# Kernel tuning notes

Hardware: AMD Instinct MI355X
Metric: run time of the kernel (lower is better)

## Reference

```python
import jax, jax.numpy as jnp
import numpy as np

B, N, D = 2, 512, 64
LN_EPS = 1e-5
NEG_SLOPE = 0.01  # torch nn.LeakyReLU default


def _layer_norm(x, g, b):
    m = jnp.mean(x, axis=-1, keepdims=True)
    v = jnp.mean(jnp.square(x - m), axis=-1, keepdims=True)
    return (x - m) * jax.lax.rsqrt(v + LN_EPS) * g + b


def setup_inputs() -> dict:
    key = jax.random.key(0)
    k0, k1, k2 = jax.random.split(key, 3)
    return {
        "ua": jax.random.normal(k0, (B, N, D), dtype=jnp.float32),
        "iid": jax.random.normal(k1, (B, 1, 1, D), dtype=jnp.float32),
        "ln_g": jnp.ones((D,), dtype=jnp.float32),
        "ln_b": jnp.zeros((D,), dtype=jnp.float32),
        "w_att": (jax.random.normal(k2, (3 * D, 1), dtype=jnp.float32)
                  / np.sqrt(3 * D).astype(np.float32)),
        "b_att": jnp.zeros((1,), dtype=jnp.float32),
    }


def reference(ua, iid, ln_g, ln_b, w_att, b_att):
    b, n, d = ua.shape
    # all-pairs expand: query[b,i,j,:] = ua[b,i,:], key[b,i,j,:] = ua[b,j,:]
    query = jnp.broadcast_to(ua[:, :, None, :], (b, n, n, d))
    key = jnp.broadcast_to(ua[:, None, :, :], (b, n, n, d))
    value = query * key
    iid_e = jnp.broadcast_to(iid, (b, n, n, d))
    wq = _layer_norm(query, ln_g, ln_b)
    wk = _layer_norm(key, ln_g, ln_b)
    wiid = _layer_norm(iid_e, ln_g, ln_b)
    qk = jnp.concatenate((wq, wk, wiid), axis=-1)  # [b,n,n,3d]
    qk = qk @ w_att + b_att                        # [b,n,n,1]
    qk = jax.nn.leaky_relu(qk, NEG_SLOPE)
    # dropout in eval mode -> identity
    scores = jnp.squeeze(qk, axis=-1)              # [b,n,n]
    alphas = jax.nn.softmax(scores, axis=-1)       # softmax over keys j
    alphas = jnp.broadcast_to(alphas[..., None], value.shape)
    return (alphas, value)
```

## Files before the change

kernel.cpp:

```cpp
#include <hip/hip_runtime.h>

#define BB 2
#define NN 512
#define DD 64
#define LN_EPS 1e-5f
#define NEG_SLOPE 0.01f

typedef float f32x4 __attribute__((ext_vector_type(4)));

__device__ __forceinline__ float wave_reduce_sum(float v) {
    #pragma unroll
    for (int off = 32; off >= 1; off >>= 1)
        v += __shfl_xor(v, off, 64);
    return v;
}

__device__ __forceinline__ float wave_reduce_max(float v) {
    #pragma unroll
    for (int off = 32; off >= 1; off >>= 1)
        v = fmaxf(v, __shfl_xor(v, off, 64));
    return v;
}

__global__ __launch_bounds__(64) void precompute_kernel(
    const float* __restrict__ ua,
    const float* __restrict__ iid,
    const float* __restrict__ ln_g,
    const float* __restrict__ ln_b,
    const float* __restrict__ w_att,
    const float* __restrict__ b_att,
    float* __restrict__ sq,
    float* __restrict__ sk,
    float* __restrict__ cb) {
    const int bid = blockIdx.x;
    const int lane = threadIdx.x;

    const float g = ln_g[lane];
    const float bet = ln_b[lane];

    if (bid < BB * NN) {
        float x = ua[bid * DD + lane];
        float m = wave_reduce_sum(x) * (1.0f / DD);
        float xc = x - m;
        float var = wave_reduce_sum(xc * xc) * (1.0f / DD);
        float r = rsqrtf(var + LN_EPS);
        float w = xc * r * g + bet;
        float s1 = wave_reduce_sum(w * w_att[lane]);
        float s2 = wave_reduce_sum(w * w_att[DD + lane]);
        if (lane == 0) {
            sq[bid] = s1;
            sk[bid] = s2;
        }
    } else {
        int b = bid - BB * NN;
        float x = iid[b * DD + lane];
        float m = wave_reduce_sum(x) * (1.0f / DD);
        float xc = x - m;
        float var = wave_reduce_sum(xc * xc) * (1.0f / DD);
        float r = rsqrtf(var + LN_EPS);
        float w = xc * r * g + bet;
        float s3 = wave_reduce_sum(w * w_att[2 * DD + lane]);
        if (lane == 0) {
            cb[b] = s3 + b_att[0];
        }
    }
}

__global__ __launch_bounds__(256) void write_kernel(
    const float* __restrict__ ua,
    const float* __restrict__ sq,
    const float* __restrict__ sk,
    const float* __restrict__ cb,
    float* __restrict__ out0,
    float* __restrict__ out1) {
    __shared__ float alpha_sh[256];
    __shared__ float red_mx[4];
    __shared__ float red_sm[4];

    const int bid2 = blockIdx.x;
    const int row  = bid2 >> 1;
    const int half = bid2 & 1;
    const int b = row >> 9;
    const int i = row & (NN - 1);
    const int tid = threadIdx.x;

    const float sqi = sq[row];
    const float c = cb[b];

    float s0 = sqi + sk[b * NN + tid] + c;
    float s1 = sqi + sk[b * NN + tid + 256] + c;
    s0 = fmaxf(s0, NEG_SLOPE * s0);
    s1 = fmaxf(s1, NEG_SLOPE * s1);

    float mx = fmaxf(s0, s1);
    mx = wave_reduce_max(mx);
    const int wid = tid >> 6;
    if ((tid & 63) == 0) red_mx[wid] = mx;
    __syncthreads();
    mx = fmaxf(fmaxf(red_mx[0], red_mx[1]), fmaxf(red_mx[2], red_mx[3]));

    float e0 = __expf(s0 - mx);
    float e1 = __expf(s1 - mx);
    float sm = wave_reduce_sum(e0 + e1);
    if ((tid & 63) == 0) red_sm[wid] = sm;
    __syncthreads();
    sm = red_sm[0] + red_sm[1] + red_sm[2] + red_sm[3];
    const float inv = 1.0f / sm;

    alpha_sh[tid] = (half ? e1 : e0) * inv;
    __syncthreads();

    const f32x4* __restrict__ uaB = (const f32x4*)(ua + (size_t)b * NN * DD);
    const f32x4* __restrict__ uaH = uaB + (size_t)half * 256 * 16;

    f32x4* __restrict__ o0 =
        (f32x4*)(out0 + (size_t)row * NN * DD + (size_t)half * 256 * DD);
    f32x4* __restrict__ o1 =
        (f32x4*)(out1 + (size_t)row * NN * DD + (size_t)half * 256 * DD);

    if (tid < 128) {
        const int l = tid;
        #pragma unroll 4
        for (int k = 0; k < 32; ++k) {
            const int idx = l + k * 128;
            const float a = alpha_sh[idx >> 4];
            f32x4 av;
            av.x = a; av.y = a; av.z = a; av.w = a;
            o0[idx] = av;
        }
    } else {
        const int l = tid - 128;
        const f32x4 ui = uaB[(size_t)i * 16 + (l & 15)];
        #pragma unroll 4
        for (int k = 0; k < 32; ++k) {
            const int idx = l + k * 128;
            const f32x4 uj = uaH[idx];
            o1[idx] = ui * uj;
        }
    }
}

extern "C" void kernel_launch(void* const* d_in, const int* in_sizes, int n_in,
                              void* d_out, int out_size, void* d_ws, size_t ws_size,
                              hipStream_t stream) {
    const float* ua    = (const float*)d_in[0];
    const float* iid   = (const float*)d_in[1];
    const float* ln_g  = (const float*)d_in[2];
    const float* ln_b  = (const float*)d_in[3];
    const float* w_att = (const float*)d_in[4];
    const float* b_att = (const float*)d_in[5];

    float* out0 = (float*)d_out;
    float* out1 = out0 + (size_t)BB * NN * NN * DD;

    float* sq = (float*)d_ws;
    float* sk = sq + BB * NN;
    float* cb = sk + BB * NN;

    precompute_kernel<<<BB * NN + BB, 64, 0, stream>>>(ua, iid, ln_g, ln_b,
                                                       w_att, b_att, sq, sk, cb);
    write_kernel<<<BB * NN * 2, 256, 0, stream>>>(ua, sq, sk, cb, out0, out1);
}
```

Before: 50.48 us.

## Fold LayerNorm precompute into value-writing kernel and split alpha writes out

The small per-row LayerNorm/score precompute is merged into a new value kernel that also writes the query*key value output with all 256 threads. The alpha softmax broadcast moves to a separate second kernel that writes only out0, again using all 256 threads. This is meant to overlap the tiny precompute with the bulk value stores and to keep each kernel's store loop uniform instead of split between thread halves. Total output traffic is unchanged, and the precompute branch makes the first wave of each block slightly unbalanced.

Result: faster. 49.04 us (median of 2 runs) (-2.9%).

```diff
diff --git a/kernel.cpp b/kernel.cpp
--- a/kernel.cpp
+++ b/kernel.cpp
@@ -22,7 +22,7 @@
     return v;
 }
 
-__global__ __launch_bounds__(64) void precompute_kernel(
+__global__ __launch_bounds__(256) void value_kernel(
     const float* __restrict__ ua,
     const float* __restrict__ iid,
     const float* __restrict__ ln_g,
@@ -31,57 +31,75 @@
     const float* __restrict__ b_att,
     float* __restrict__ sq,
     float* __restrict__ sk,
-    float* __restrict__ cb) {
-    const int bid = blockIdx.x;
-    const int lane = threadIdx.x;
+    float* __restrict__ cb,
+    float* __restrict__ out1) {
+    const int bid2 = blockIdx.x;
+    const int tid = threadIdx.x;
 
-    const float g = ln_g[lane];
-    const float bet = ln_b[lane];
+    if (tid < 64 && bid2 < BB * NN + BB) {
+        const int lane = tid;
+        const float g = ln_g[lane];
+        const float bet = ln_b[lane];
+        if (bid2 < BB * NN) {
+            float x = ua[bid2 * DD + lane];
+            float m = wave_reduce_sum(x) * (1.0f / DD);
+            float xc = x - m;
+            float var = wave_reduce_sum(xc * xc) * (1.0f / DD);
+            float r = rsqrtf(var + LN_EPS);
+            float w = xc * r * g + bet;
+            float s1 = wave_reduce_sum(w * w_att[lane]);
+            float s2 = wave_reduce_sum(w * w_att[DD + lane]);
+            if (lane == 0) {
+                sq[bid2] = s1;
+                sk[bid2] = s2;
+            }
+        } else {
+            int b = bid2 - BB * NN;
+            float x = iid[b * DD + lane];
+            float m = wave_reduce_sum(x) * (1.0f / DD);
+            float xc = x - m;
+            float var = wave_reduce_sum(xc * xc) * (1.0f / DD);
+            float r = rsqrtf(var + LN_EPS);
+            float w = xc * r * g + bet;
+            float s3 = wave_reduce_sum(w * w_att[2 * DD + lane]);
+            if (lane == 0) {
+                cb[b] = s3 + b_att[0];
+            }
+        }
+    }
 
-    if (bid < BB * NN) {
-        float x = ua[bid * DD + lane];
-        float m = wave_reduce_sum(x) * (1.0f / DD);
-        float xc = x - m;
-        float var = wave_reduce_sum(xc * xc) * (1.0f / DD);
-        float r = rsqrtf(var + LN_EPS);
-        float w = xc * r * g + bet;
-        float s1 = wave_reduce_sum(w * w_att[lane]);
-        float s2 = wave_reduce_sum(w * w_att[DD + lane]);
-        if (lane == 0) {
-            sq[bid] = s1;
-            sk[bid] = s2;
-        }
-    } else {
-        int b = bid - BB * NN;
-        float x = iid[b * DD + lane];
-        float m = wave_reduce_sum(x) * (1.0f / DD);
-        float xc = x - m;
-        float var = wave_reduce_sum(xc * xc) * (1.0f / DD);
-        float r = rsqrtf(var + LN_EPS);
-        float w = xc * r * g + bet;
-        float s3 = wave_reduce_sum(w * w_att[2 * DD + lane]);
-        if (lane == 0) {
-            cb[b] = s3 + b_att[0];
-        }
+    const int row = bid2 >> 1;
+    const int half = bid2 & 1;
+    const int b = row >> 9;
+    const int i = row & (NN - 1);
+
+    const f32x4* __restrict__ uaB = (const f32x4*)(ua + (size_t)b * NN * DD);
+    const f32x4* __restrict__ uaH = uaB + (size_t)half * 256 * 16;
+    const f32x4 ui = uaB[(size_t)i * 16 + (tid & 15)];
+
+    f32x4* __restrict__ o1 =
+        (f32x4*)(out1 + (size_t)row * NN * DD + (size_t)half * 256 * DD);
+
+    #pragma unroll 4
+    for (int k = 0; k < 16; ++k) {
+        const int idx = tid + k * 256;
+        o1[idx] = ui * uaH[idx];
     }
 }
 
-__global__ __launch_bounds__(256) void write_kernel(
-    const float* __restrict__ ua,
+__global__ __launch_bounds__(256) void alpha_kernel(
     const float* __restrict__ sq,
     const float* __restrict__ sk,
     const float* __restrict__ cb,
-    float* __restrict__ out0,
-    float* __restrict__ out1) {
+    float* __restrict__ out0) {
     __shared__ float alpha_sh[256];
     __shared__ float red_mx[4];
     __shared__ float red_sm[4];
 
     const int bid2 = blockIdx.x;
-    const int row  = bid2 >> 1;
+    const int row = bid2 >> 1;
     const int half = bid2 & 1;
     const int b = row >> 9;
-    const int i = row & (NN - 1);
     const int tid = threadIdx.x;
 
     const float sqi = sq[row];
@@ -99,8 +117,8 @@
     __syncthreads();
     mx = fmaxf(fmaxf(red_mx[0], red_mx[1]), fmaxf(red_mx[2], red_mx[3]));
 
-    float e0 = __expf(s0 - mx);
-    float e1 = __expf(s1 - mx);
+    const float e0 = __expf(s0 - mx);
+    const float e1 = __expf(s1 - mx);
     float sm = wave_reduce_sum(e0 + e1);
     if ((tid & 63) == 0) red_sm[wid] = sm;
     __syncthreads();
@@ -110,33 +128,16 @@
     alpha_sh[tid] = (half ? e1 : e0) * inv;
     __syncthreads();
 
-    const f32x4* __restrict__ uaB = (const f32x4*)(ua + (size_t)b * NN * DD);
-    const f32x4* __restrict__ uaH = uaB + (size_t)half * 256 * 16;
-
     f32x4* __restrict__ o0 =
         (f32x4*)(out0 + (size_t)row * NN * DD + (size_t)half * 256 * DD);
-    f32x4* __restrict__ o1 =
-        (f32x4*)(out1 + (size_t)row * NN * DD + (size_t)half * 256 * DD);
 
-    if (tid < 128) {
-        const int l = tid;
-        #pragma unroll 4
-        for (int k = 0; k < 32; ++k) {
-            const int idx = l + k * 128;
-            const float a = alpha_sh[idx >> 4];
-            f32x4 av;
-            av.x = a; av.y = a; av.z = a; av.w = a;
-            o0[idx] = av;
-        }
-    } else {
-        const int l = tid - 128;
-        const f32x4 ui = uaB[(size_t)i * 16 + (l & 15)];
-        #pragma unroll 4
-        for (int k = 0; k < 32; ++k) {
-            const int idx = l + k * 128;
-            const f32x4 uj = uaH[idx];
-            o1[idx] = ui * uj;
-        }
+    #pragma unroll 4
+    for (int k = 0; k < 16; ++k) {
+        const int idx = tid + k * 256;
+        const float a = alpha_sh[idx >> 4];
+        f32x4 av;
+        av.x = a; av.y = a; av.z = a; av.w = a;
+        o0[idx] = av;
     }
 }
 
@@ -157,7 +158,7 @@
     float* sk = sq + BB * NN;
     float* cb = sk + BB * NN;
 
-    precompute_kernel<<<BB * NN + BB, 64, 0, stream>>>(ua, iid, ln_g, ln_b,
-                                                       w_att, b_att, sq, sk, cb);
-    write_kernel<<<BB * NN * 2, 256, 0, stream>>>(ua, sq, sk, cb, out0, out1);
+    value_kernel<<<BB * NN * 2, 256, 0, stream>>>(ua, iid, ln_g, ln_b,
+                                                  w_att, b_att, sq, sk, cb, out1);
+    alpha_kernel<<<BB * NN * 2, 256, 0, stream>>>(sq, sk, cb, out0);
 }
```
